# Kernel tuning notes

Hardware: AMD Instinct MI355X
Metric: run time of the kernel (lower is better)

The kernel has to match this reference:

```python
import jax, jax.numpy as jnp
import numpy as np

B, T1, T2, D, H = 16, 512, 64, 768, 12
E = D // H  # head dim


def _proj(x, W, b):
    # x: [B,T,D], W: [6,D,D], b: [6,D] -> [6,B,H,T,E], scaled by E**-0.25 (applied to q,k,v alike, per source)
    t = x.shape[1]
    p = jnp.einsum('btd,kdf->kbtf', x, W) + b[:, None, None, :]
    p = p.reshape(6, B, t, H, E).transpose(0, 1, 3, 2, 4)
    return p * (E ** -0.25)


def setup_inputs() -> dict:
    key = jax.random.key(0)
    ks = jax.random.split(key, 12)
    s = 0.02
    return {
        'feats': jax.random.normal(ks[0], (B, T1, D), jnp.float32),
        'inps': jax.random.normal(ks[1], (B, T2, D), jnp.float32),
        'att_mask': jax.random.randint(ks[2], (B, 1, 1, T1 + T2), 0, 2).astype(bool),
        'W_f': s * jax.random.normal(ks[3], (6, D, D), jnp.float32),
        'b_f': s * jax.random.normal(ks[4], (6, D), jnp.float32),
        'W_i': s * jax.random.normal(ks[5], (6, D, D), jnp.float32),
        'b_i': s * jax.random.normal(ks[6], (6, D), jnp.float32),
        'Wu_v': s * jax.random.normal(ks[7], (D, D), jnp.float32),
        'bu_v': s * jax.random.normal(ks[8], (D,), jnp.float32),
        'Wu_l': s * jax.random.normal(ks[9], (D, D), jnp.float32),
        'bu_l': s * jax.random.normal(ks[10], (D,), jnp.float32),
    }


def reference(feats, inps, att_mask, W_f, b_f, W_i, b_i, Wu_v, bu_v, Wu_l, bu_l):
    NEG = jnp.float32(-1e9)
    # projections from feats: [keys_v_v, queries_v_v, values_v_v, queries_l_v, keys_v_l, values_v_l]
    k_vv, q_vv, v_vv, q_lv, k_vl, v_vl = _proj(feats, W_f, b_f)
    # projections from inps: [keys_l_v, values_l_v, queries_v_l, queries_l_l, keys_l_l, values_l_l]
    k_lv, v_lv, q_vl, q_ll, k_ll, v_ll = _proj(inps, W_i, b_i)

    # visual stream: two distinct queries over the two key blocks, joint softmax over t1+t2
    dot_vv = jnp.einsum('bhqe,bhke->bhqk', q_vv, k_vv)   # [B,H,T1,T1]
    dot_lv = jnp.einsum('bhqe,bhke->bhqk', q_lv, k_lv)   # [B,H,T1,T2]
    att_v = jnp.concatenate([dot_vv, dot_lv], axis=-1)    # [B,H,T1,T1+T2]
    att_v = jax.nn.softmax(jnp.where(att_mask, NEG, att_v), axis=-1)
    vals_v = jnp.concatenate([v_vv, v_lv], axis=2)        # [B,H,T1+T2,E]
    out_v = jnp.einsum('bhqk,bhke->bhqe', att_v, vals_v)
    out_v = out_v.transpose(0, 2, 1, 3).reshape(B, T1, D)
    out_v = out_v @ Wu_v + bu_v

    # language stream
    dot_vl = jnp.einsum('bhqe,bhke->bhqk', q_vl, k_vl)    # [B,H,T2,T1]
    dot_ll = jnp.einsum('bhqe,bhke->bhqk', q_ll, k_ll)    # [B,H,T2,T2]
    att_l = jnp.concatenate([dot_vl, dot_ll], axis=-1)    # [B,H,T2,T1+T2]
    att_l = jax.nn.softmax(jnp.where(att_mask, NEG, att_l), axis=-1)
    vals_l = jnp.concatenate([v_vl, v_ll], axis=2)        # [B,H,T1+T2,E]
    out_l = jnp.einsum('bhqk,bhke->bhqe', att_l, vals_l)
    out_l = out_l.transpose(0, 2, 1, 3).reshape(B, T2, D)
    out_l = out_l @ Wu_l + bu_l

    return (out_v, out_l)
```

## Files before the change

### kernel.cpp

```cpp
#include <hip/hip_runtime.h>
#include <stdint.h>

#define BB 16
#define T1C 512
#define T2C 64
#define DC 768
#define HC 12
#define EC 64
#define SC 576
#define QSCALE 0.35355339059327379f

typedef __attribute__((ext_vector_type(8))) short bf16x8;
typedef __attribute__((ext_vector_type(4))) float f32x4;

__device__ __forceinline__ uint16_t f2b(float f) {
    union { float f; uint32_t i; } v; v.f = f;
    return (uint16_t)((v.i + 0x7fffu + ((v.i >> 16) & 1u)) >> 16);
}
__device__ __forceinline__ uint16_t f2bfast(float f) {
    union { float f; uint32_t i; } v; v.f = f;
    return (uint16_t)((v.i + 0x8000u) >> 16);
}
__device__ __forceinline__ uint32_t pk2(float a, float b) {
    return (uint32_t)f2b(a) | ((uint32_t)f2b(b) << 16);
}

__device__ __forceinline__ void gll16(const void* g, void* l) {
    __builtin_amdgcn_global_load_lds(
        (const __attribute__((address_space(1))) uint32_t*)(uintptr_t)g,
        (__attribute__((address_space(3))) uint32_t*)(uintptr_t)l, 16, 0, 0);
}

__global__ void detect(const uint32_t* __restrict__ mw, int* __restrict__ flags) {
    __shared__ int aW, aB, aL;
    if (threadIdx.x == 0) { aW = 0; aB = 0; aL = 0; }
    __syncthreads();
    int lW = 0, lB = 0, lL = 0;
    for (int i = threadIdx.x; i < 2304; i += 256) {
        uint32_t w = mw[i];
        if (w > 1u) lW = 1;
        if (((w) & 0xffu) > 1u || ((w >> 8) & 0xffu) > 1u ||
            ((w >> 16) & 0xffu) > 1u || ((w >> 24) & 0xffu) > 1u) lB = 1;
        if ((w & 0xffffu) > 1u) lL = 1;
    }
    if (lW) atomicOr(&aW, 1);
    if (lB) atomicOr(&aB, 1);
    if (lL) atomicOr(&aL, 1);
    __syncthreads();
    if (threadIdx.x == 0)
        flags[0] = (!aW) ? 0 : ((!aB) ? 1 : (aL ? 2 : 0));
}

__global__ __launch_bounds__(256) void wtrans(
    const float* __restrict__ Wf, const float* __restrict__ Wi,
    const float* __restrict__ Wuv, const float* __restrict__ Wul,
    uint16_t* __restrict__ Wt)
{
    __shared__ float tile[32][33];
    const int z = blockIdx.z;
    const float* src = (z < 6)  ? Wf + (size_t)z * DC * DC
                     : (z < 12) ? Wi + (size_t)(z - 6) * DC * DC
                     : (z == 12 ? Wuv : Wul);
    uint16_t* dst = Wt + (size_t)z * DC * DC;
    const int tx = threadIdx.x & 31, ty = threadIdx.x >> 5;
    const int k0 = blockIdx.x * 32, f0 = blockIdx.y * 32;
#pragma unroll
    for (int r = 0; r < 4; r++)
        tile[ty + r * 8][tx] = src[(size_t)(k0 + ty + r * 8) * DC + f0 + tx];
    __syncthreads();
#pragma unroll
    for (int r = 0; r < 4; r++)
        dst[(size_t)(f0 + ty + r * 8) * DC + k0 + tx] = f2b(tile[tx][ty + r * 8]);
}

__global__ __launch_bounds__(256) void xswz(
    const float* __restrict__ Xf, const float* __restrict__ Xi,
    uint16_t* __restrict__ Of, uint16_t* __restrict__ Oi)
{
    const int nf = BB * T1C * DC / 8;
    const int ni = BB * T2C * DC / 8;
    int t = blockIdx.x * 256 + threadIdx.x;
    const float* src; uint16_t* dst; int cc;
    if (t < nf) { src = Xf; dst = Of; cc = t; }
    else        { cc = t - nf; if (cc >= ni) return; src = Xi; dst = Oi; }
    int rlid = cc & 15;
    int t2 = cc >> 4;
    int qd = t2 & 3;
    int t3 = t2 >> 2;
    int kt = t3 % 24;
    int p  = t3 / 24;
    const float* sp = src + (size_t)(p * 16 + rlid) * DC + kt * 32 + qd * 8;
    float4 a = *(const float4*)sp;
    float4 b = *(const float4*)(sp + 4);
    uint4 o;
    o.x = pk2(a.x, a.y); o.y = pk2(a.z, a.w);
    o.z = pk2(b.x, b.y); o.w = pk2(b.z, b.w);
    *(uint4*)(dst + (size_t)cc * 8) = o;
}

#define BSTR 76

__global__ __launch_bounds__(256, 3) void gemm_proj_mfma(
    const uint16_t* __restrict__ Xsf, const uint16_t* __restrict__ Xsi,
    const uint16_t* __restrict__ Wt,
    const float* __restrict__ b_f, const float* __restrict__ b_i,
    uint16_t* __restrict__ Pf, uint16_t* __restrict__ Pi)
{
    __shared__ union {
        uint16_t B[128 * 32];
        uint16_t bounce[4][16 * BSTR];
    } sm;
    const int tid = threadIdx.x;
    const int w = tid >> 6, l = tid & 63;
    const bool isf = (blockIdx.x < 64);
    const int mx = isf ? blockIdx.x : blockIdx.x - 64;
    const int m0 = mx * 128;
    const int T  = isf ? T1C : T2C;
    const uint16_t* Xs = isf ? Xsf : Xsi;
    const float* bias  = isf ? b_f : b_i;
    uint16_t* P        = isf ? Pf : Pi;
    const int vmask    = isf ? 0x24 : 0x22;
    const int k6 = blockIdx.y / 6, nt = blockIdx.y % 6;
    const int n0 = nt * 128;
    const uint16_t* Bsrc = Wt + (size_t)((isf ? 0 : 6) + k6) * DC * DC;

    const int lid = l & 15, qd = l >> 4;
    const int wm = w >> 1, wn = w & 1;
    const int br = l >> 2, bk = (l & 3) * 8;
    const int p0 = mx * 8 + wm * 4;

    f32x4 acc[4][4] = {};

    for (int kt = 0; kt < DC / 32; ++kt) {
        __syncthreads();
#pragma unroll
        for (int n = 0; n < 2; ++n) {
            int c = w * 2 + n;
            gll16(Bsrc + (size_t)(n0 + c * 16 + br) * DC + kt * 32 + bk, &sm.B[c * 512]);
        }
        bf16x8 af[4];
#pragma unroll
        for (int i = 0; i < 4; i++)
            af[i] = *(const bf16x8*)(Xs + ((size_t)((p0 + i) * 24 + kt) * 64 + l) * 8);
        __syncthreads();
        bf16x8 bf[4];
#pragma unroll
        for (int j = 0; j < 4; j++)
            bf[j] = *(const bf16x8*)&sm.B[(wn * 64 + j * 16 + lid) * 32 + qd * 8];
#pragma unroll
        for (int i = 0; i < 4; i++)
#pragma unroll
            for (int j = 0; j < 4; j++)
                acc[i][j] = __builtin_amdgcn_mfma_f32_16x16x32_bf16(af[i], bf[j], acc[i][j], 0, 0, 0);
    }

    float bv[4];
#pragma unroll
    for (int j = 0; j < 4; j++)
        bv[j] = bias[k6 * DC + n0 + wn * 64 + j * 16 + lid];
    __syncthreads();

    uint16_t* reg = sm.bounce[w];
    const int mb = m0 + wm * 64;
    const int b = mb / T, tb = mb - b * T;
    const int h = nt * 2 + wn;
    const int rrow = l >> 2;
    const int rcol = (l & 3) * 16;

    if (!((vmask >> k6) & 1)) {
        uint16_t* dst0 = P + ((((size_t)k6 * BB + b) * HC + h) * T + tb + rrow) * EC + rcol;
#pragma unroll
        for (int p = 0; p < 4; p++) {
#pragma unroll
            for (int j = 0; j < 4; j++)
#pragma unroll
                for (int r = 0; r < 4; r++)
                    reg[(qd * 4 + r) * BSTR + j * 16 + lid] =
                        f2b((acc[p][j][r] + bv[j]) * QSCALE);
            uint4 d0 = *(const uint4*)&reg[rrow * BSTR + rcol];
            uint4 d1 = *(const uint4*)&reg[rrow * BSTR + rcol + 8];
            uint16_t* dst = dst0 + (size_t)p * 16 * EC;
            *(uint4*)dst = d0;
            *(uint4*)(dst + 8) = d1;
        }
    } else {
        uint16_t* dst0 = P + (size_t)k6 * BB * HC * T * EC
                           + (((size_t)b * HC + h) * EC + rrow) * T + tb + rcol;
#pragma unroll
        for (int p = 0; p < 4; p++) {
#pragma unroll
            for (int i = 0; i < 4; i++) {
                uint32_t w0 = pk2((acc[i][p][0] + bv[p]) * QSCALE,
                                  (acc[i][p][1] + bv[p]) * QSCALE);
                uint32_t w1 = pk2((acc[i][p][2] + bv[p]) * QSCALE,
                                  (acc[i][p][3] + bv[p]) * QSCALE);
                *(uint2*)&reg[lid * BSTR + i * 16 + qd * 4] = make_uint2(w0, w1);
            }
            uint4 d0 = *(const uint4*)&reg[rrow * BSTR + rcol];
            uint4 d1 = *(const uint4*)&reg[rrow * BSTR + rcol + 8];
            uint16_t* dst = dst0 + (size_t)p * 16 * T;
            *(uint4*)dst = d0;
            *(uint4*)(dst + 8) = d1;
        }
    }
}

__global__ __launch_bounds__(256, 3) void gemm_out_mfma(
    const uint16_t* __restrict__ Osv, const uint16_t* __restrict__ Osl,
    const uint16_t* __restrict__ Wt,
    const float* __restrict__ bu_v, const float* __restrict__ bu_l,
    float* __restrict__ out)
{
    __shared__ uint16_t Bs[128 * 32];
    const int tid = threadIdx.x;
    const int w = tid >> 6, l = tid & 63;
    const bool isv = (blockIdx.x < 64);
    const int mx = isv ? blockIdx.x : blockIdx.x - 64;
    const int m0 = mx * 128;
    const int rowoff = isv ? 0 : BB * T1C;
    const uint16_t* A = isv ? Osv : Osl;
    const uint16_t* Wtm = Wt + (size_t)(isv ? 12 : 13) * DC * DC;
    const float* bias = isv ? bu_v : bu_l;
    const int n0 = blockIdx.y * 128;
    const int lid = l & 15, qd = l >> 4;
    const int wm = w >> 1, wn = w & 1;
    const int br = l >> 2, bk = (l & 3) * 8;
    const int p0 = mx * 8 + wm * 4;

    f32x4 acc[4][4] = {};

    for (int kt = 0; kt < DC / 32; ++kt) {
        __syncthreads();
#pragma unroll
        for (int n = 0; n < 2; ++n) {
            int c = w * 2 + n;
            gll16(Wtm + (size_t)(n0 + c * 16 + br) * DC + kt * 32 + bk, &Bs[c * 512]);
        }
        bf16x8 af[4];
#pragma unroll
        for (int i = 0; i < 4; i++)
            af[i] = *(const bf16x8*)(A + ((size_t)((p0 + i) * 24 + kt) * 64 + l) * 8);
        __syncthreads();
        bf16x8 bf[4];
#pragma unroll
        for (int j = 0; j < 4; j++)
            bf[j] = *(const bf16x8*)&Bs[(wn * 64 + j * 16 + lid) * 32 + qd * 8];
#pragma unroll
        for (int i = 0; i < 4; i++)
#pragma unroll
            for (int j = 0; j < 4; j++)
                acc[i][j] = __builtin_amdgcn_mfma_f32_16x16x32_bf16(af[i], bf[j], acc[i][j], 0, 0, 0);
    }

    float bv[4];
#pragma unroll
    for (int j = 0; j < 4; j++)
        bv[j] = bias[n0 + wn * 64 + j * 16 + lid];
#pragma unroll
    for (int i = 0; i < 4; i++)
#pragma unroll
        for (int j = 0; j < 4; j++)
#pragma unroll
            for (int r = 0; r < 4; r++) {
                int m = m0 + wm * 64 + i * 16 + qd * 4 + r;
                int f = n0 + wn * 64 + j * 16 + lid;
                out[(size_t)(rowoff + m) * DC + f] = acc[i][j][r] + bv[j];
            }
}

__global__ __launch_bounds__(256, 3) void attn_mfma(
    const uint16_t* __restrict__ Pf,
    const uint16_t* __restrict__ Pi,
    const void* __restrict__ maskp,
    const int* __restrict__ flags,
    uint16_t* __restrict__ Osv,
    uint16_t* __restrict__ Osl)
{
    __shared__ uint16_t Klds[64 * 72];
    __shared__ uint16_t Vlds[64 * 72];
    __shared__ uint16_t Plds[4][16 * 72];
    __shared__ float    Ma[SC];
    __shared__ float    Lw[4][16];

    const int bh = blockIdx.x;
    const int tile = blockIdx.y;
    const int b = bh / HC, h = bh % HC;
    const int tid = threadIdx.x;
    const int w = tid >> 6, l = tid & 63;
    const int lid = l & 15, qd = l >> 4;

    const size_t SF = (size_t)BB * HC * T1C * EC;
    const size_t SI = (size_t)BB * HC * T2C * EC;

    const bool vis = (tile < 8);
    const uint16_t *Qa, *Qb, *K1, *K2, *V1, *V2;
    uint16_t* O; int Tq, q0;
    if (vis) { Qa = Pf + 1 * SF; Qb = Pf + 3 * SF; K1 = Pf;          K2 = Pi;
               V1 = Pf + 2 * SF; V2 = Pi + 1 * SI; O = Osv; Tq = T1C; q0 = tile * 64; }
    else     { Qa = Pi + 2 * SI; Qb = Pi + 3 * SI; K1 = Pf + 4 * SF; K2 = Pi + 4 * SI;
               V1 = Pf + 5 * SF; V2 = Pi + 5 * SI; O = Osl; Tq = T2C; q0 = 0; }

    {
        const int kind = flags[0];
        for (int i = tid; i < SC; i += 256) {
            int idx = b * SC + i;
            int mv;
            if (kind == 0)      mv = ((const uint32_t*)maskp)[idx] != 0u;
            else if (kind == 1) mv = ((const uint8_t*)maskp)[idx] != 0;
            else                mv = ((const uint16_t*)maskp)[idx] != 0;
            Ma[i] = mv ? -1e9f : 0.0f;
        }
    }

    const int q = q0 + w * 16 + lid;
    const uint16_t* Qrow = Qa + ((size_t)bh * Tq + q) * EC;
    bf16x8 qf0 = *(const bf16x8*)(Qrow + qd * 8);
    bf16x8 qf1 = *(const bf16x8*)(Qrow + 32 + qd * 8);

    f32x4 o[4];
#pragma unroll
    for (int ef = 0; ef < 4; ef++) { o[ef][0]=0.f; o[ef][1]=0.f; o[ef][2]=0.f; o[ef][3]=0.f; }
    float u[4] = {0.f, 0.f, 0.f, 0.f};

    const int skey = tid >> 2, se0 = (tid & 3) * 16;
    const int ve = tid >> 2,  vc = tid & 3;

    for (int c = 0; c < 9; ++c) {
        const uint16_t *Ksrc, *Vbase; int Tkv, kofs;
        if (c < 8) {
            Ksrc = K1 + ((size_t)bh * T1C + c * 64) * EC;
            Vbase = V1 + (size_t)bh * EC * T1C; Tkv = T1C; kofs = c * 64;
        } else {
            Ksrc = K2 + (size_t)bh * T2C * EC;
            Vbase = V2 + (size_t)bh * EC * T2C; Tkv = T2C; kofs = 0;
            const uint16_t* Qrow2 = Qb + ((size_t)bh * Tq + q) * EC;
            qf0 = *(const bf16x8*)(Qrow2 + qd * 8);
            qf1 = *(const bf16x8*)(Qrow2 + 32 + qd * 8);
        }
        __syncthreads();
        *(uint4*)&Klds[skey * 72 + se0]     = *(const uint4*)(Ksrc + skey * EC + se0);
        *(uint4*)&Klds[skey * 72 + se0 + 8] = *(const uint4*)(Ksrc + skey * EC + se0 + 8);
#pragma unroll
        for (int g = 0; g < 2; g++) {
            int key0 = vc * 16 + g * 8;
            *(uint4*)&Vlds[ve * 72 + key0] =
                *(const uint4*)(Vbase + (size_t)ve * Tkv + kofs + key0);
        }
        __syncthreads();

        const int k0 = c * 64;
        f32x4 s[4];
#pragma unroll
        for (int sub = 0; sub < 4; sub++) {
            bf16x8 kf0 = *(const bf16x8*)&Klds[(sub * 16 + lid) * 72 + qd * 8];
            bf16x8 kf1 = *(const bf16x8*)&Klds[(sub * 16 + lid) * 72 + 32 + qd * 8];
            f32x4 z; z[0]=0.f; z[1]=0.f; z[2]=0.f; z[3]=0.f;
            z = __builtin_amdgcn_mfma_f32_16x16x32_bf16(qf0, kf0, z, 0, 0, 0);
            s[sub] = __builtin_amdgcn_mfma_f32_16x16x32_bf16(qf1, kf1, z, 0, 0, 0);
        }
#pragma unroll
        for (int sub = 0; sub < 4; sub++) {
            float mv = Ma[k0 + sub * 16 + lid];
#pragma unroll
            for (int r = 0; r < 4; r++) {
                float p = __expf(s[sub][r] + mv);
                u[r] += p;
                Plds[w][(qd * 4 + r) * 72 + sub * 16 + lid] = f2bfast(p);
            }
        }
#pragma unroll
        for (int half = 0; half < 2; half++) {
            bf16x8 pf = *(const bf16x8*)&Plds[w][lid * 72 + half * 32 + qd * 8];
#pragma unroll
            for (int ef = 0; ef < 4; ef++) {
                bf16x8 vf = *(const bf16x8*)&Vlds[(ef * 16 + lid) * 72 + half * 32 + qd * 8];
                o[ef] = __builtin_amdgcn_mfma_f32_16x16x32_bf16(vf, pf, o[ef], 0, 0, 0);
            }
        }
    }

#pragma unroll
    for (int d = 1; d <= 8; d <<= 1)
#pragma unroll
        for (int r = 0; r < 4; r++)
            u[r] += __shfl_xor(u[r], d, 64);
    if (lid == 0) {
#pragma unroll
        for (int r = 0; r < 4; r++) Lw[w][qd * 4 + r] = u[r];
    }
    float rl = 1.f / Lw[w][lid];

    const size_t p = ((size_t)b * Tq + q0 + w * 16) >> 4;
#pragma unroll
    for (int ef = 0; ef < 4; ef++) {
        uint32_t w0 = pk2(o[ef][0] * rl, o[ef][1] * rl);
        uint32_t w1 = pk2(o[ef][2] * rl, o[ef][3] * rl);
        size_t chunk = ((p * 24 + h * 2 + (ef >> 1)) * 4 + (ef & 1) * 2 + (qd >> 1)) * 16 + lid;
        *(uint2*)(O + chunk * 8 + (qd & 1) * 4) = make_uint2(w0, w1);
    }
}

extern "C" void kernel_launch(void* const* d_in, const int* in_sizes, int n_in,
                              void* d_out, int out_size, void* d_ws, size_t ws_size,
                              hipStream_t stream)
{
    const float* feats = (const float*)d_in[0];
    const float* inps  = (const float*)d_in[1];
    const void*  maskp = d_in[2];
    const float* W_f   = (const float*)d_in[3];
    const float* b_f   = (const float*)d_in[4];
    const float* W_i   = (const float*)d_in[5];
    const float* b_i   = (const float*)d_in[6];
    const float* Wu_v  = (const float*)d_in[7];
    const float* bu_v  = (const float*)d_in[8];
    const float* Wu_l  = (const float*)d_in[9];
    const float* bu_l  = (const float*)d_in[10];

    const size_t MAT = (size_t)DC * DC;
    const size_t PF_E = 6ull * BB * HC * T1C * EC;
    const size_t PI_E = 6ull * BB * HC * T2C * EC;
    uint16_t* Wt  = (uint16_t*)d_ws;
    uint16_t* Osv = Wt;
    uint16_t* Osl = Wt + (size_t)BB * T1C * HC * EC;
    uint16_t* Pf  = Wt + 14 * MAT;
    uint16_t* Pi  = Pf + PF_E;
    int* flags    = (int*)(Pi + PI_E);

    uint16_t* Xsf = (uint16_t*)d_out;
    uint16_t* Xsi = Xsf + (size_t)BB * T1C * DC;

    detect<<<dim3(1), dim3(256), 0, stream>>>((const uint32_t*)maskp, flags);

    wtrans<<<dim3(24, 24, 14), dim3(256), 0, stream>>>(W_f, W_i, Wu_v, Wu_l, Wt);

    {
        int nchunks = (BB * T1C * DC + BB * T2C * DC) / 8;
        xswz<<<dim3((nchunks + 255) / 256), dim3(256), 0, stream>>>(feats, inps, Xsf, Xsi);
    }

    gemm_proj_mfma<<<dim3(72, 36), dim3(256), 0, stream>>>(
        Xsf, Xsi, Wt, b_f, b_i, Pf, Pi);

    attn_mfma<<<dim3(BB * HC, 9), dim3(256), 0, stream>>>(
        Pf, Pi, maskp, flags, Osv, Osl);

    gemm_out_mfma<<<dim3(72, 6), dim3(256), 0, stream>>>(
        Osv, Osl, Wt, bu_v, bu_l, (float*)d_out);
}
```

Before: 269.5 us.

## Triple-buffer projection GEMM with LDS-staged A/B tiles and 256-row blocks

Rewrites the projection GEMM to use 512-thread blocks with 256x128 tiles and BK=64, staging both A and B into LDS via direct global-to-LDS loads with XOR swizzle and a three-stage buffer ring. Loads for tile k+2 are issued in two halves interleaved with the MFMA phases, with explicit vmcnt waits, barriers and priority hints. The input conversion kernel becomes a plain row-major fp32-to-bf16 cast since A is no longer read in a pre-swizzled fragment layout. This targets global load latency and poor reuse of A. In exchange it uses much more LDS (about 144KB), which limits occupancy, and the block count halves along M.

Result: slower. 285.2 us (+5.8%).

```diff
diff --git a/kernel.cpp b/kernel.cpp
--- a/kernel.cpp
+++ b/kernel.cpp
@@ -73,50 +73,46 @@
         dst[(size_t)(f0 + ty + r * 8) * DC + k0 + tx] = f2b(tile[tx][ty + r * 8]);
 }
 
-__global__ __launch_bounds__(256) void xswz(
+__global__ __launch_bounds__(256) void xcvt(
     const float* __restrict__ Xf, const float* __restrict__ Xi,
     uint16_t* __restrict__ Of, uint16_t* __restrict__ Oi)
 {
     const int nf = BB * T1C * DC / 8;
     const int ni = BB * T2C * DC / 8;
     int t = blockIdx.x * 256 + threadIdx.x;
-    const float* src; uint16_t* dst; int cc;
-    if (t < nf) { src = Xf; dst = Of; cc = t; }
-    else        { cc = t - nf; if (cc >= ni) return; src = Xi; dst = Oi; }
-    int rlid = cc & 15;
-    int t2 = cc >> 4;
-    int qd = t2 & 3;
-    int t3 = t2 >> 2;
-    int kt = t3 % 24;
-    int p  = t3 / 24;
-    const float* sp = src + (size_t)(p * 16 + rlid) * DC + kt * 32 + qd * 8;
+    const float* src; uint16_t* dst; int c;
+    if (t < nf) { src = Xf; dst = Of; c = t; }
+    else        { c = t - nf; if (c >= ni) return; src = Xi; dst = Oi; }
+    const float* sp = src + (size_t)c * 8;
     float4 a = *(const float4*)sp;
     float4 b = *(const float4*)(sp + 4);
     uint4 o;
     o.x = pk2(a.x, a.y); o.y = pk2(a.z, a.w);
     o.z = pk2(b.x, b.y); o.w = pk2(b.z, b.w);
-    *(uint4*)(dst + (size_t)cc * 8) = o;
+    *(uint4*)(dst + (size_t)c * 8) = o;
 }
 
 #define BSTR 76
 
-__global__ __launch_bounds__(256, 3) void gemm_proj_mfma(
-    const uint16_t* __restrict__ Xsf, const uint16_t* __restrict__ Xsi,
+__global__ __launch_bounds__(512, 2) void gemm_proj_mfma(
+    const uint16_t* __restrict__ Xbf, const uint16_t* __restrict__ Xbi,
     const uint16_t* __restrict__ Wt,
     const float* __restrict__ b_f, const float* __restrict__ b_i,
     uint16_t* __restrict__ Pf, uint16_t* __restrict__ Pi)
 {
     __shared__ union {
-        uint16_t B[128 * 32];
-        uint16_t bounce[4][16 * BSTR];
+        struct { uint16_t A[3][256 * 64]; uint16_t B[3][128 * 64]; } st;
+        uint16_t bounce[8][16 * BSTR];
     } sm;
+
     const int tid = threadIdx.x;
     const int w = tid >> 6, l = tid & 63;
-    const bool isf = (blockIdx.x < 64);
-    const int mx = isf ? blockIdx.x : blockIdx.x - 64;
-    const int m0 = mx * 128;
+    const int lid = l & 15, qd = l >> 4;
+    const bool isf = (blockIdx.x < 32);
+    const int mx = isf ? blockIdx.x : blockIdx.x - 32;
+    const int m0 = mx * 256;
     const int T  = isf ? T1C : T2C;
-    const uint16_t* Xs = isf ? Xsf : Xsi;
+    const uint16_t* Xb = isf ? Xbf : Xbi;
     const float* bias  = isf ? b_f : b_i;
     uint16_t* P        = isf ? Pf : Pi;
     const int vmask    = isf ? 0x24 : 0x22;
@@ -124,41 +120,107 @@
     const int n0 = nt * 128;
     const uint16_t* Bsrc = Wt + (size_t)((isf ? 0 : 6) + k6) * DC * DC;
 
-    const int lid = l & 15, qd = l >> 4;
     const int wm = w >> 1, wn = w & 1;
-    const int br = l >> 2, bk = (l & 3) * 8;
-    const int p0 = mx * 8 + wm * 4;
+
+    const uint16_t* aSrc[4];
+#pragma unroll
+    for (int i = 0; i < 4; ++i) {
+        int g = i * 512 + tid, r = g >> 3, p = g & 7, cc = p ^ (r & 7);
+        aSrc[i] = Xb + (size_t)(m0 + r) * DC + cc * 8;
+    }
+    const uint16_t* bSrc2[2];
+#pragma unroll
+    for (int i = 0; i < 2; ++i) {
+        int g = i * 512 + tid, r = g >> 3, p = g & 7, cc = p ^ (r & 7);
+        bSrc2[i] = Bsrc + (size_t)(n0 + r) * DC + cc * 8;
+    }
+
+    uint32_t aOff[2][4], bOff[2][4];
+#pragma unroll
+    for (int kk = 0; kk < 2; ++kk)
+#pragma unroll
+        for (int i = 0; i < 4; ++i) {
+            int ra = wm * 64 + i * 16 + lid;
+            int rb = wn * 64 + i * 16 + lid;
+            uint32_t sl = (uint32_t)(((kk * 4 + qd) ^ (lid & 7)) * 16);
+            aOff[kk][i] = (uint32_t)ra * 128 + sl;
+            bOff[kk][i] = (uint32_t)rb * 128 + sl;
+        }
+
+#define STG_A(tk, bu, i) gll16(aSrc[i] + (tk) * 64, (uint16_t*)sm.st.A[bu] + (size_t)((i) * 512 + w * 64) * 8)
+#define STG_B(tk, bu, i) gll16(bSrc2[i] + (tk) * 64, (uint16_t*)sm.st.B[bu] + (size_t)((i) * 512 + w * 64) * 8)
+#define AFRAG(bu, kk, i) (*(const bf16x8*)((const char*)sm.st.A[bu] + aOff[kk][i]))
+#define BFRAG(bu, kk, j) (*(const bf16x8*)((const char*)sm.st.B[bu] + bOff[kk][j]))
+
+    STG_A(0, 0, 0); STG_A(0, 0, 1); STG_A(0, 0, 2); STG_A(0, 0, 3);
+    STG_B(0, 0, 0); STG_B(0, 0, 1);
+    STG_A(1, 1, 0); STG_A(1, 1, 1); STG_A(1, 1, 2); STG_A(1, 1, 3);
+    STG_B(1, 1, 0); STG_B(1, 1, 1);
+    asm volatile("s_waitcnt vmcnt(6)" ::: "memory");
+    __builtin_amdgcn_s_barrier();
+    asm volatile("" ::: "memory");
+    __builtin_amdgcn_sched_barrier(0);
 
     f32x4 acc[4][4] = {};
 
-    for (int kt = 0; kt < DC / 32; ++kt) {
-        __syncthreads();
-#pragma unroll
-        for (int n = 0; n < 2; ++n) {
-            int c = w * 2 + n;
-            gll16(Bsrc + (size_t)(n0 + c * 16 + br) * DC + kt * 32 + bk, &sm.B[c * 512]);
-        }
-        bf16x8 af[4];
-#pragma unroll
-        for (int i = 0; i < 4; i++)
-            af[i] = *(const bf16x8*)(Xs + ((size_t)((p0 + i) * 24 + kt) * 64 + l) * 8);
-        __syncthreads();
-        bf16x8 bf[4];
-#pragma unroll
-        for (int j = 0; j < 4; j++)
-            bf[j] = *(const bf16x8*)&sm.B[(wn * 64 + j * 16 + lid) * 32 + qd * 8];
-#pragma unroll
-        for (int i = 0; i < 4; i++)
-#pragma unroll
-            for (int j = 0; j < 4; j++)
-                acc[i][j] = __builtin_amdgcn_mfma_f32_16x16x32_bf16(af[i], bf[j], acc[i][j], 0, 0, 0);
-    }
+#pragma unroll
+    for (int kt = 0; kt < 12; ++kt) {
+        const int cb = kt % 3, sb = (kt + 2) % 3;
+
+        if (kt < 10) { STG_A(kt + 2, sb, 0); STG_A(kt + 2, sb, 1); STG_B(kt + 2, sb, 0); }
+        {
+            bf16x8 a0[4], b0[4];
+#pragma unroll
+            for (int i = 0; i < 4; ++i) a0[i] = AFRAG(cb, 0, i);
+#pragma unroll
+            for (int j = 0; j < 4; ++j) b0[j] = BFRAG(cb, 0, j);
+            __builtin_amdgcn_s_barrier();
+            asm volatile("s_waitcnt lgkmcnt(0)" ::: "memory");
+            __builtin_amdgcn_sched_barrier(0);
+            __builtin_amdgcn_s_setprio(1);
+#pragma unroll
+            for (int i = 0; i < 4; ++i)
+#pragma unroll
+                for (int j = 0; j < 4; ++j)
+                    acc[i][j] = __builtin_amdgcn_mfma_f32_16x16x32_bf16(a0[i], b0[j], acc[i][j], 0, 0, 0);
+            __builtin_amdgcn_s_setprio(0);
+            __builtin_amdgcn_sched_barrier(0);
+            __builtin_amdgcn_s_barrier();
+            asm volatile("" ::: "memory");
+            __builtin_amdgcn_sched_barrier(0);
+        }
+
+        if (kt < 10) { STG_A(kt + 2, sb, 2); STG_A(kt + 2, sb, 3); STG_B(kt + 2, sb, 1); }
+        {
+            bf16x8 a1[4], b1[4];
+#pragma unroll
+            for (int i = 0; i < 4; ++i) a1[i] = AFRAG(cb, 1, i);
+#pragma unroll
+            for (int j = 0; j < 4; ++j) b1[j] = BFRAG(cb, 1, j);
+            __builtin_amdgcn_s_barrier();
+            asm volatile("s_waitcnt lgkmcnt(0)" ::: "memory");
+            __builtin_amdgcn_sched_barrier(0);
+            __builtin_amdgcn_s_setprio(1);
+#pragma unroll
+            for (int i = 0; i < 4; ++i)
+#pragma unroll
+                for (int j = 0; j < 4; ++j)
+                    acc[i][j] = __builtin_amdgcn_mfma_f32_16x16x32_bf16(a1[i], b1[j], acc[i][j], 0, 0, 0);
+            __builtin_amdgcn_s_setprio(0);
+            __builtin_amdgcn_sched_barrier(0);
+            if (kt < 10)       { asm volatile("s_waitcnt vmcnt(6)" ::: "memory"); }
+            else if (kt == 10) { asm volatile("s_waitcnt vmcnt(0)" ::: "memory"); }
+            __builtin_amdgcn_s_barrier();
+            asm volatile("" ::: "memory");
+            __builtin_amdgcn_sched_barrier(0);
+        }
+    }
+    __syncthreads();
 
     float bv[4];
 #pragma unroll
-    for (int j = 0; j < 4; j++)
+    for (int j = 0; j < 4; ++j)
         bv[j] = bias[k6 * DC + n0 + wn * 64 + j * 16 + lid];
-    __syncthreads();
 
     uint16_t* reg = sm.bounce[w];
     const int mb = m0 + wm * 64;
@@ -203,6 +265,10 @@
             *(uint4*)(dst + 8) = d1;
         }
     }
+#undef STG_A
+#undef STG_B
+#undef AFRAG
+#undef BFRAG
 }
 
 __global__ __launch_bounds__(256, 3) void gemm_out_mfma(
@@ -426,8 +492,8 @@
     uint16_t* Pi  = Pf + PF_E;
     int* flags    = (int*)(Pi + PI_E);
 
-    uint16_t* Xsf = (uint16_t*)d_out;
-    uint16_t* Xsi = Xsf + (size_t)BB * T1C * DC;
+    uint16_t* Xbf = (uint16_t*)d_out;
+    uint16_t* Xbi = Xbf + (size_t)BB * T1C * DC;
 
     detect<<<dim3(1), dim3(256), 0, stream>>>((const uint32_t*)maskp, flags);
 
@@ -435,11 +501,11 @@
 
     {
         int nchunks = (BB * T1C * DC + BB * T2C * DC) / 8;
-        xswz<<<dim3((nchunks + 255) / 256), dim3(256), 0, stream>>>(feats, inps, Xsf, Xsi);
-    }
-
-    gemm_proj_mfma<<<dim3(72, 36), dim3(256), 0, stream>>>(
-        Xsf, Xsi, Wt, b_f, b_i, Pf, Pi);
+        xcvt<<<dim3((nchunks + 255) / 256), dim3(256), 0, stream>>>(feats, inps, Xbf, Xbi);
+    }
+
+    gemm_proj_mfma<<<dim3(36, 36), dim3(512), 0, stream>>>(
+        Xbf, Xbi, Wt, b_f, b_i, Pf, Pi);
 
     attn_mfma<<<dim3(BB * HC, 9), dim3(256), 0, stream>>>(
         Pf, Pi, maskp, flags, Osv, Osl);
```

## Triple-buffer projection GEMM weight tiles in swizzled LDS with two-ahead prefetch

Applied to the files above, without the earlier changes.

The projection GEMM now stages weight tiles with a K depth of 64 in three rotating LDS buffers, prefetching two iterations ahead with direct global-to-LDS loads. This leaves one barrier per iteration, down from two per 32-wide K step, and overlaps loads with MFMA work. An XOR swizzle on the LDS column layout is added to avoid bank conflicts on the fragment reads. The LDS footprint grows to about 48KB per block, which may limit occupancy at 3 blocks per CU. Correctness also depends on implicit vmcnt ordering before the barrier.

After: 280.6 us. 4.1% more time.

```diff
diff --git a/kernel.cpp b/kernel.cpp
--- a/kernel.cpp
+++ b/kernel.cpp
@@ -107,7 +107,7 @@
     uint16_t* __restrict__ Pf, uint16_t* __restrict__ Pi)
 {
     __shared__ union {
-        uint16_t B[128 * 32];
+        uint16_t B[3][128 * 64];
         uint16_t bounce[4][16 * BSTR];
     } sm;
     const int tid = threadIdx.x;
@@ -126,39 +126,75 @@
 
     const int lid = l & 15, qd = l >> 4;
     const int wm = w >> 1, wn = w & 1;
-    const int br = l >> 2, bk = (l & 3) * 8;
     const int p0 = mx * 8 + wm * 4;
 
+    const int r8 = l >> 3;
+    const int scol = (l & 7) ^ r8;
+    const uint16_t* bsrc[4];
+    uint32_t bdst[4];
+#pragma unroll
+    for (int i = 0; i < 4; ++i) {
+        bsrc[i] = Bsrc + (size_t)(n0 + (i * 4 + w) * 8 + r8) * DC + scol * 8;
+        bdst[i] = (uint32_t)(i * 4 + w) * 512;
+    }
+    uint32_t boff[2][4];
+#pragma unroll
+    for (int kk = 0; kk < 2; ++kk)
+#pragma unroll
+        for (int j = 0; j < 4; ++j) {
+            int row = wn * 64 + j * 16 + lid;
+            boff[kk][j] = (uint32_t)row * 64 + (uint32_t)((((kk * 4 + qd) ^ (lid & 7))) * 8);
+        }
+
     f32x4 acc[4][4] = {};
 
-    for (int kt = 0; kt < DC / 32; ++kt) {
-        __syncthreads();
-#pragma unroll
-        for (int n = 0; n < 2; ++n) {
-            int c = w * 2 + n;
-            gll16(Bsrc + (size_t)(n0 + c * 16 + br) * DC + kt * 32 + bk, &sm.B[c * 512]);
-        }
-        bf16x8 af[4];
-#pragma unroll
-        for (int i = 0; i < 4; i++)
-            af[i] = *(const bf16x8*)(Xs + ((size_t)((p0 + i) * 24 + kt) * 64 + l) * 8);
-        __syncthreads();
-        bf16x8 bf[4];
-#pragma unroll
-        for (int j = 0; j < 4; j++)
-            bf[j] = *(const bf16x8*)&sm.B[(wn * 64 + j * 16 + lid) * 32 + qd * 8];
-#pragma unroll
-        for (int i = 0; i < 4; i++)
-#pragma unroll
-            for (int j = 0; j < 4; j++)
-                acc[i][j] = __builtin_amdgcn_mfma_f32_16x16x32_bf16(af[i], bf[j], acc[i][j], 0, 0, 0);
-    }
+#pragma unroll
+    for (int i = 0; i < 4; ++i) gll16(bsrc[i],      &sm.B[0][bdst[i]]);
+#pragma unroll
+    for (int i = 0; i < 4; ++i) gll16(bsrc[i] + 64, &sm.B[1][bdst[i]]);
+    asm volatile("s_waitcnt vmcnt(4)" ::: "memory");
+    __builtin_amdgcn_s_barrier();
+    __builtin_amdgcn_sched_barrier(0);
+
+#pragma unroll
+    for (int ktt = 0; ktt < 12; ++ktt) {
+        const int cb = ktt % 3;
+        bf16x8 af[2][4];
+#pragma unroll
+        for (int kk = 0; kk < 2; ++kk)
+#pragma unroll
+            for (int i = 0; i < 4; ++i)
+                af[kk][i] = *(const bf16x8*)(Xs +
+                    ((size_t)((p0 + i) * 24 + ktt * 2 + kk) * 64 + l) * 8);
+        if (ktt < 10) {
+            const int sb = (ktt + 2) % 3;
+#pragma unroll
+            for (int i = 0; i < 4; ++i)
+                gll16(bsrc[i] + (ktt + 2) * 64, &sm.B[sb][bdst[i]]);
+        }
+#pragma unroll
+        for (int kk = 0; kk < 2; ++kk) {
+            bf16x8 bq[4];
+#pragma unroll
+            for (int j = 0; j < 4; ++j)
+                bq[j] = *(const bf16x8*)&sm.B[cb][boff[kk][j]];
+#pragma unroll
+            for (int i = 0; i < 4; ++i)
+#pragma unroll
+                for (int j = 0; j < 4; ++j)
+                    acc[i][j] = __builtin_amdgcn_mfma_f32_16x16x32_bf16(
+                        af[kk][i], bq[j], acc[i][j], 0, 0, 0);
+        }
+        __builtin_amdgcn_sched_barrier(0);
+        __builtin_amdgcn_s_barrier();
+        __builtin_amdgcn_sched_barrier(0);
+    }
+    __syncthreads();
 
     float bv[4];
 #pragma unroll
     for (int j = 0; j < 4; j++)
         bv[j] = bias[k6 * DC + n0 + wn * 64 + j * 16 + lid];
-    __syncthreads();
 
     uint16_t* reg = sm.bounce[w];
     const int mb = m0 + wm * 64;
```

## Register-prefetch next K/V chunk during attention compute and hoist second Q load

Applied to the files above, without the earlier changes.

The attention loop now loads the next chunk's K and V tiles from global memory into registers while the current chunk is being computed. Each iteration stores the already-fetched registers into LDS between raw barriers with explicit waitcnt and sched_barrier fences. The second query fragment is loaded once before the loop instead of inside the last iteration, and the loop is fully unrolled. This hides global load latency behind the MFMA work, at the cost of extra VGPRs that may reduce occupancy.

After: 270.6 us. Within noise of the previous version (+0.4%).

```diff
diff --git a/kernel.cpp b/kernel.cpp
--- a/kernel.cpp
+++ b/kernel.cpp
@@ -313,9 +313,12 @@
     }
 
     const int q = q0 + w * 16 + lid;
-    const uint16_t* Qrow = Qa + ((size_t)bh * Tq + q) * EC;
+    const uint16_t* Qrow  = Qa + ((size_t)bh * Tq + q) * EC;
+    const uint16_t* Qrow2 = Qb + ((size_t)bh * Tq + q) * EC;
     bf16x8 qf0 = *(const bf16x8*)(Qrow + qd * 8);
     bf16x8 qf1 = *(const bf16x8*)(Qrow + 32 + qd * 8);
+    bf16x8 qg0 = *(const bf16x8*)(Qrow2 + qd * 8);
+    bf16x8 qg1 = *(const bf16x8*)(Qrow2 + 32 + qd * 8);
 
     f32x4 o[4];
 #pragma unroll
@@ -325,38 +328,51 @@
     const int skey = tid >> 2, se0 = (tid & 3) * 16;
     const int ve = tid >> 2,  vc = tid & 3;
 
+    auto kptr = [&](int c) -> const uint16_t* {
+        return (c < 8) ? K1 + ((size_t)bh * T1C + c * 64 + skey) * EC + se0
+                       : K2 + ((size_t)bh * T2C + skey) * EC + se0;
+    };
+    auto vptr = [&](int c) -> const uint16_t* {
+        return (c < 8) ? V1 + ((size_t)bh * EC + ve) * T1C + c * 64 + vc * 16
+                       : V2 + ((size_t)bh * EC + ve) * T2C + vc * 16;
+    };
+
+    uint4 ka0 = *(const uint4*)kptr(0);
+    uint4 ka1 = *(const uint4*)(kptr(0) + 8);
+    uint4 va0 = *(const uint4*)vptr(0);
+    uint4 va1 = *(const uint4*)(vptr(0) + 8);
+
+#pragma unroll
     for (int c = 0; c < 9; ++c) {
-        const uint16_t *Ksrc, *Vbase; int Tkv, kofs;
+        uint4 kb0, kb1, vb0, vb1;
         if (c < 8) {
-            Ksrc = K1 + ((size_t)bh * T1C + c * 64) * EC;
-            Vbase = V1 + (size_t)bh * EC * T1C; Tkv = T1C; kofs = c * 64;
-        } else {
-            Ksrc = K2 + (size_t)bh * T2C * EC;
-            Vbase = V2 + (size_t)bh * EC * T2C; Tkv = T2C; kofs = 0;
-            const uint16_t* Qrow2 = Qb + ((size_t)bh * Tq + q) * EC;
-            qf0 = *(const bf16x8*)(Qrow2 + qd * 8);
-            qf1 = *(const bf16x8*)(Qrow2 + 32 + qd * 8);
-        }
-        __syncthreads();
-        *(uint4*)&Klds[skey * 72 + se0]     = *(const uint4*)(Ksrc + skey * EC + se0);
-        *(uint4*)&Klds[skey * 72 + se0 + 8] = *(const uint4*)(Ksrc + skey * EC + se0 + 8);
-#pragma unroll
-        for (int g = 0; g < 2; g++) {
-            int key0 = vc * 16 + g * 8;
-            *(uint4*)&Vlds[ve * 72 + key0] =
-                *(const uint4*)(Vbase + (size_t)ve * Tkv + kofs + key0);
-        }
-        __syncthreads();
+            kb0 = *(const uint4*)kptr(c + 1);
+            kb1 = *(const uint4*)(kptr(c + 1) + 8);
+            vb0 = *(const uint4*)vptr(c + 1);
+            vb1 = *(const uint4*)(vptr(c + 1) + 8);
+        }
+        __builtin_amdgcn_s_barrier();
+        __builtin_amdgcn_sched_barrier(0);
+        *(uint4*)&Klds[skey * 72 + se0]         = ka0;
+        *(uint4*)&Klds[skey * 72 + se0 + 8]     = ka1;
+        *(uint4*)&Vlds[ve * 72 + vc * 16]       = va0;
+        *(uint4*)&Vlds[ve * 72 + vc * 16 + 8]   = va1;
+        asm volatile("s_waitcnt lgkmcnt(0)" ::: "memory");
+        __builtin_amdgcn_sched_barrier(0);
+        __builtin_amdgcn_s_barrier();
+        __builtin_amdgcn_sched_barrier(0);
 
         const int k0 = c * 64;
+        const bf16x8 q_0 = (c < 8) ? qf0 : qg0;
+        const bf16x8 q_1 = (c < 8) ? qf1 : qg1;
         f32x4 s[4];
 #pragma unroll
         for (int sub = 0; sub < 4; sub++) {
             bf16x8 kf0 = *(const bf16x8*)&Klds[(sub * 16 + lid) * 72 + qd * 8];
             bf16x8 kf1 = *(const bf16x8*)&Klds[(sub * 16 + lid) * 72 + 32 + qd * 8];
             f32x4 z; z[0]=0.f; z[1]=0.f; z[2]=0.f; z[3]=0.f;
-            z = __builtin_amdgcn_mfma_f32_16x16x32_bf16(qf0, kf0, z, 0, 0, 0);
-            s[sub] = __builtin_amdgcn_mfma_f32_16x16x32_bf16(qf1, kf1, z, 0, 0, 0);
+            z = __builtin_amdgcn_mfma_f32_16x16x32_bf16(q_0, kf0, z, 0, 0, 0);
+            s[sub] = __builtin_amdgcn_mfma_f32_16x16x32_bf16(q_1, kf1, z, 0, 0, 0);
         }
 #pragma unroll
         for (int sub = 0; sub < 4; sub++) {
@@ -377,6 +393,7 @@
                 o[ef] = __builtin_amdgcn_mfma_f32_16x16x32_bf16(vf, pf, o[ef], 0, 0, 0);
             }
         }
+        if (c < 8) { ka0 = kb0; ka1 = kb1; va0 = vb0; va1 = vb1; }
     }
 
 #pragma unroll
```
